# Kernel optimization log

Hardware: AMD Instinct MI355X
Metric: run time of the kernel (lower is better)

Reference implementation:

```python
import jax, jax.numpy as jnp
import numpy as np
from jax import lax

B, L, D = 2, 4096, 2048
K, KQ, M, H = 32, 4, 8, 8  # H = D*expand // (K*M)
MEM = K * H              # 256
FLAT = K * H * M         # 2048
CONV_W = 4
DIM_SWIGLU = H * 3 * 2   # out_expand_factor=3 -> 48
N_DECAY = K - 4          # 28 decay heads, 4 anchor heads


def setup_inputs() -> dict:
    key = jax.random.key(0)
    ks = jax.random.split(key, 8)
    x = jax.random.normal(ks[0], (B, L, D), dtype=jnp.float32)
    W_mem = jax.random.normal(ks[1], (D, MEM + K), dtype=jnp.float32) / np.sqrt(D)
    conv_k = jax.random.normal(ks[2], (CONV_W, 1, MEM + K), dtype=jnp.float32) * 0.3
    W_q = jax.random.normal(ks[3], (D, KQ * H * M * 2), dtype=jnp.float32) / np.sqrt(D)
    theta = jnp.asarray(np.tile(np.geomspace(0.001, 3.0, M).reshape(1, 1, 1, 1, M),
                                (1, 1, K, H, 1)), dtype=jnp.float32)
    decay_slopes = jnp.asarray(np.log(np.expm1(np.geomspace(0.001, 0.1, N_DECAY))), dtype=jnp.float32)
    anchor_slopes = jnp.asarray(np.log(np.expm1(np.geomspace(0.01, 0.1, 4))), dtype=jnp.float32)
    score_scale = jnp.ones((K,), dtype=jnp.float32)
    g = np.sqrt(2.0 / (H + DIM_SWIGLU))
    W_re = jax.random.normal(ks[4], (K, H, DIM_SWIGLU), dtype=jnp.float32) * g
    W_im = jax.random.normal(ks[5], (K, H, DIM_SWIGLU), dtype=jnp.float32) * g
    norm_scale = jnp.ones((1, 1, K, H), dtype=jnp.float32)
    W_out = jax.random.normal(ks[6], (K * H * 3, D), dtype=jnp.float32) / np.sqrt(K * H * 3)
    return {"x": x, "W_mem": W_mem, "conv_k": conv_k, "W_q": W_q, "theta": theta,
            "decay_slopes": decay_slopes, "anchor_slopes": anchor_slopes,
            "score_scale": score_scale, "W_re": W_re, "W_im": W_im,
            "norm_scale": norm_scale, "W_out": W_out}


def _forward(x, W_mem, conv_k, W_q, theta, decay_slopes, anchor_slopes,
             score_scale, W_re, W_im, norm_scale, W_out):
    b, l, d = x.shape
    # memory branch: dense + causal depthwise conv
    z = x @ W_mem  # (b, l, MEM+K)
    z = lax.conv_general_dilated(z, conv_k, window_strides=(1,),
                                 padding=[(CONV_W - 1, 0)],
                                 dimension_numbers=('NHC', 'HIO', 'NHC'),
                                 feature_group_count=MEM + K)
    k_val = z[..., :MEM].reshape(b, l, K, H)
    s_raw = z[..., MEM:].reshape(b, l, K, 1)
    # query branch
    q = (x @ W_q).reshape(b, l, KQ, H, M, 2)
    q_re, q_im = q[..., 0], q[..., 1]
    # per-head time weights (decay heads look back from end, anchor heads from start)
    pos = jnp.arange(l, dtype=jnp.float32)
    slopes_d = jax.nn.softplus(decay_slopes).reshape(1, 1, -1, 1)
    slopes_a = jax.nn.softplus(anchor_slopes).reshape(1, 1, -1, 1)
    dist = jnp.maximum(jnp.float32(l - 1) - pos, 0.0)
    log_w = jnp.concatenate([-slopes_d * dist[None, :, None, None],
                             -slopes_a * pos[None, :, None, None]], axis=2)  # (1,l,K,1)
    log_p = jnp.clip(score_scale[None, None, :, None] * s_raw, -20.0, 20.0)
    p_w = jnp.exp(log_p + log_w)  # (b,l,K,1)
    # complex rotation of keys
    phi = k_val[..., None] * theta          # (b,l,K,H,M)
    re_k, im_k = jnp.cos(phi), jnp.sin(phi)
    pw5 = p_w[..., None]
    merged = jnp.concatenate([p_w.squeeze(-1),
                              (pw5 * re_k).reshape(b, l, FLAT),
                              (pw5 * im_k).reshape(b, l, FLAT)], axis=-1)
    cs = jnp.cumsum(merged, axis=1)
    den = cs[..., :K]                       # (b,l,K)
    num_re = cs[..., K:K + FLAT]
    num_im = cs[..., K + FLAT:]
    inv_den = 1.0 / jnp.maximum(den[..., None], 1e-4)  # (b,l,K,1)
    state_re = num_re.reshape(b, l, K, H, M) * inv_den[..., None]
    state_im = num_im.reshape(b, l, K, H, M) * inv_den[..., None]
    # GQA-style query repeat
    n_rep = K // KQ
    q_re = jnp.repeat(q_re, n_rep, axis=2)
    q_im = jnp.repeat(q_im, n_rep, axis=2)
    out_re = jnp.sum(state_re * q_re + state_im * q_im, axis=-1)  # (b,l,K,H)
    out_im = jnp.sum(state_im * q_re - state_re * q_im, axis=-1)
    out_re = out_re * norm_scale
    out_im = out_im * norm_scale
    y = jnp.einsum('blkh,khn->blkn', out_re, W_re) + jnp.einsum('blkh,khn->blkn', out_im, W_im)
    y_val, y_gate = jnp.split(y, 2, axis=-1)
    y = (y_val * jax.nn.silu(y_gate)).reshape(b, l, -1)
    return y @ W_out


def reference(x, W_mem, conv_k, W_q, theta, decay_slopes, anchor_slopes,
              score_scale, W_re, W_im, norm_scale, W_out):
    return _forward(x, W_mem, conv_k, W_q, theta, decay_slopes, anchor_slopes,
                    score_scale, W_re, W_im, norm_scale, W_out)
```

## Files before the change

kernel.cpp:

```cpp
#include <hip/hip_runtime.h>
#include <hip/hip_bf16.h>
#include <math.h>

#define BB 2
#define LL 4096
#define DD 2048
#define KK 32
#define MEM 256
#define CTOT 288
#define NQ 512
#define ZSTR 800
#define NPAD 896
#define FLAT 2048
#define CMERG 4128
#define CH 16
#define NCH 256
#define YDIM 768
#define KV2 1536
#define BL (BB*LL)

typedef __attribute__((ext_vector_type(4))) float f32x4;
typedef __attribute__((ext_vector_type(8))) short bf16x8;
typedef __attribute__((ext_vector_type(8))) unsigned short u16x8;

__device__ inline unsigned short f2b(float v) {
    __hip_bfloat16 h = __float2bfloat16(v);
    return *reinterpret_cast<unsigned short*>(&h);
}
__device__ inline float b2f(unsigned short u) {
    __hip_bfloat16 h;
    *reinterpret_cast<unsigned short*>(&h) = u;
    return __bfloat162float(h);
}

__device__ inline void gload16(const void* g, void* l) {
    __builtin_amdgcn_global_load_lds(
        (const __attribute__((address_space(1))) unsigned int*)g,
        (__attribute__((address_space(3))) unsigned int*)l, 16, 0, 0);
}

template<int HH>
__device__ inline float bcast8(float v) {
    return __int_as_float(__builtin_amdgcn_ds_swizzle(__float_as_int(v), (HH << 5) | 0x18));
}

__device__ inline float fast_sigmoid_mul(float val, float g) {
    return val * __builtin_amdgcn_rcpf(1.f + __expf(-g));
}

__global__ __launch_bounds__(256) void cvt_x(const float* __restrict__ x,
                                             unsigned short* __restrict__ xb) {
    size_t i = ((size_t)blockIdx.x * 256 + threadIdx.x) * 8;
    float4 a = *(const float4*)&x[i];
    float4 b = *(const float4*)&x[i + 4];
    u16x8 o;
    o[0] = f2b(a.x); o[1] = f2b(a.y); o[2] = f2b(a.z); o[3] = f2b(a.w);
    o[4] = f2b(b.x); o[5] = f2b(b.y); o[6] = f2b(b.z); o[7] = f2b(b.w);
    *(u16x8*)&xb[i] = o;
}

__global__ __launch_bounds__(256) void prep_wb(const float* __restrict__ W_mem,
                                               const float* __restrict__ W_q,
                                               unsigned short* __restrict__ Wb) {
    int n = blockIdx.x;
    for (int k = threadIdx.x; k < DD; k += 256) {
        float v = 0.f;
        if (n < CTOT) v = W_mem[(size_t)k * CTOT + n];
        else if (n < ZSTR) v = W_q[(size_t)k * NQ + (n - CTOT)];
        Wb[(size_t)n * DD + k] = f2b(v);
    }
}

__global__ __launch_bounds__(256) void prep_wo(const float* __restrict__ W_out,
                                               unsigned short* __restrict__ Wo) {
    int n = blockIdx.x;
    for (int k = threadIdx.x; k < YDIM; k += 256) {
        float v = W_out[(size_t)k * DD + n];
        unsigned short hi = f2b(v);
        float r = v - b2f(hi);
        Wo[(size_t)n * KV2 + k] = hi;
        Wo[(size_t)n * KV2 + YDIM + k] = f2b(r);
    }
}

template<bool CBF16>
__global__ __launch_bounds__(256) void gemm_mfma(const unsigned short* __restrict__ A,
                                                 const unsigned short* __restrict__ Bh_g,
                                                 void* __restrict__ Cout,
                                                 int Kd, int Nvalid, int Cstride) {
    __shared__ unsigned short As[2][4096];
    __shared__ unsigned short Bh[2][4096];
    int tid = threadIdx.x;
    int lane = tid & 63;
    int wave = tid >> 6;
    int wr = wave >> 1, wc = wave & 1;

    int nwg = gridDim.x * gridDim.y;
    int bid = blockIdx.y * gridDim.x + blockIdx.x;
    int cpx = nwg >> 3;
    int swz = (bid & 7) * cpx + (bid >> 3);
    int bx = swz % gridDim.x, by = swz / gridDim.x;
    int m0 = by * 128;
    int n0 = bx * 128;

    f32x4 acc[4][4];
#pragma unroll
    for (int i = 0; i < 4; ++i)
#pragma unroll
        for (int j = 0; j < 4; ++j) acc[i][j] = (f32x4){0.f, 0.f, 0.f, 0.f};

    int f0 = tid, f1 = 256 + tid;
    int row0 = f0 >> 2, ks0 = (f0 & 3) ^ ((row0 >> 1) & 3);
    int row1 = f1 >> 2, ks1 = (f1 & 3) ^ ((row1 >> 1) & 3);
    const unsigned short* ga0 = &A[(size_t)(m0 + row0) * Kd + ks0 * 8];
    const unsigned short* ga1 = &A[(size_t)(m0 + row1) * Kd + ks1 * 8];
    const unsigned short* gb0 = &Bh_g[(size_t)(n0 + row0) * Kd + ks0 * 8];
    const unsigned short* gb1 = &Bh_g[(size_t)(n0 + row1) * Kd + ks1 * 8];
    int l0 = (wave * 64) * 8;
    int l1 = (256 + wave * 64) * 8;

    int g = lane >> 4, rr = lane & 15;

#define STAGE(buf, koff) do {                                          \
        gload16(ga0 + (koff), &As[buf][l0]);                           \
        gload16(ga1 + (koff), &As[buf][l1]);                           \
        gload16(gb0 + (koff), &Bh[buf][l0]);                           \
        gload16(gb1 + (koff), &Bh[buf][l1]);                           \
    } while (0)

    STAGE(0, 0);
    __syncthreads();

    int nIter = Kd >> 5;
    int cur = 0;
    for (int it = 0; it < nIter; ++it) {
        if (it + 1 < nIter) STAGE(cur ^ 1, (it + 1) * 32);

        bf16x8 av[4], bhv[4];
#pragma unroll
        for (int i = 0; i < 4; ++i) {
            int ra = wr * 64 + i * 16 + rr;
            av[i] = *(const bf16x8*)&As[cur][ra * 32 + ((g ^ ((ra >> 1) & 3)) * 8)];
            int rb = wc * 64 + i * 16 + rr;
            bhv[i] = *(const bf16x8*)&Bh[cur][rb * 32 + ((g ^ ((rb >> 1) & 3)) * 8)];
        }
#pragma unroll
        for (int i = 0; i < 4; ++i)
#pragma unroll
            for (int j = 0; j < 4; ++j)
                acc[i][j] = __builtin_amdgcn_mfma_f32_16x16x32_bf16(av[i], bhv[j], acc[i][j], 0, 0, 0);

        __syncthreads();
        cur ^= 1;
    }
#undef STAGE

    int cg = lane >> 4, cr = lane & 15;
#pragma unroll
    for (int i = 0; i < 4; ++i)
#pragma unroll
        for (int j = 0; j < 4; ++j) {
            int colb = n0 + wc * 64 + j * 16 + cr;
            if (colb < Nvalid) {
#pragma unroll
                for (int r = 0; r < 4; ++r) {
                    int rowb = m0 + wr * 64 + i * 16 + cg * 4 + r;
                    if (CBF16)
                        ((unsigned short*)Cout)[(size_t)rowb * Cstride + colb] = f2b(acc[i][j][r]);
                    else
                        ((float*)Cout)[(size_t)rowb * Cstride + colb] = acc[i][j][r];
                }
            }
        }
}

__global__ __launch_bounds__(512, 2) void gemm256(const unsigned short* __restrict__ A,
                                                  const unsigned short* __restrict__ Bm,
                                                  float* __restrict__ C,
                                                  int KA, int Kv, int Cstride) {
    __shared__ __attribute__((aligned(16))) unsigned short As[2][16384];
    __shared__ __attribute__((aligned(16))) unsigned short Bs[2][16384];
    int tid = threadIdx.x;
    int lane = tid & 63, wave = tid >> 6;
    int wm = wave >> 2, wn = wave & 3;

    int nwg = gridDim.x * gridDim.y;
    int bid = blockIdx.y * gridDim.x + blockIdx.x;
    int cpx = nwg >> 3;
    int swz = (bid & 7) * cpx + (bid >> 3);
    int bx = swz % gridDim.x, by = swz / gridDim.x;
    int m0 = by * 256, n0 = bx * 256;

    f32x4 acc[8][4];
#pragma unroll
    for (int i = 0; i < 8; ++i)
#pragma unroll
        for (int j = 0; j < 4; ++j) acc[i][j] = (f32x4){0.f, 0.f, 0.f, 0.f};

    const unsigned short* pA[4];
    const unsigned short* pB[4];
    int ldsoff[4];
#pragma unroll
    for (int j = 0; j < 4; ++j) {
        int f = j * 512 + tid;
        int row = f >> 3, s = f & 7;
        int sg = s ^ (row & 7);
        pA[j] = A + (size_t)(m0 + row) * KA + sg * 8;
        pB[j] = Bm + (size_t)(n0 + row) * Kv + sg * 8;
        ldsoff[j] = (j * 512 + wave * 64) * 8;
    }

    int rr = lane & 15, kg = lane >> 4;

#pragma unroll
    for (int j = 0; j < 4; ++j) gload16(pB[j], &Bs[0][ldsoff[j]]);
#pragma unroll
    for (int j = 0; j < 4; ++j) gload16(pA[j], &As[0][ldsoff[j]]);
    asm volatile("s_waitcnt vmcnt(0)" ::: "memory");
    __builtin_amdgcn_s_barrier();

    int nT = Kv >> 6;
    int cur = 0;

#define LDA(fr, t) ({ int ra_ = wm * 128 + (fr) * 16 + rr;                       \
        int sd_ = (t) * 4 + kg;                                                  \
        *(const bf16x8*)&As[cur][(ra_ * 8 + (sd_ ^ (ra_ & 7))) * 8]; })
#define LDB(fc, t) ({ int rb_ = wn * 64 + (fc) * 16 + rr;                        \
        int sd_ = (t) * 4 + kg;                                                  \
        *(const bf16x8*)&Bs[cur][(rb_ * 8 + (sd_ ^ (rb_ & 7))) * 8]; })

    for (int it = 0; it < nT; ++it) {
        int nxt = cur ^ 1;
        bool hn = (it + 1 < nT);
        int k0n = (it + 1) << 6;
        int kkA = (k0n >= KA) ? (k0n - KA) : k0n;

        if (hn) {
#pragma unroll
            for (int j = 0; j < 4; ++j) gload16(pB[j] + k0n, &Bs[nxt][ldsoff[j]]);
#pragma unroll
            for (int j = 0; j < 4; ++j) gload16(pA[j] + kkA, &As[nxt][ldsoff[j]]);
        }

        bf16x8 bv[8];
#pragma unroll
        for (int j = 0; j < 4; ++j) { bv[2 * j] = LDB(j, 0); bv[2 * j + 1] = LDB(j, 1); }
#pragma unroll
        for (int i = 0; i < 8; ++i) {
            bf16x8 a0 = LDA(i, 0);
            bf16x8 a1 = LDA(i, 1);
#pragma unroll
            for (int j = 0; j < 4; ++j) {
                acc[i][j] = __builtin_amdgcn_mfma_f32_16x16x32_bf16(a0, bv[2 * j], acc[i][j], 0, 0, 0);
                acc[i][j] = __builtin_amdgcn_mfma_f32_16x16x32_bf16(a1, bv[2 * j + 1], acc[i][j], 0, 0, 0);
            }
        }

        asm volatile("s_waitcnt vmcnt(0)" ::: "memory");
        __builtin_amdgcn_s_barrier();
        cur = nxt;
    }
#undef LDA
#undef LDB

    int cg = lane >> 4;
#pragma unroll
    for (int i = 0; i < 8; ++i)
#pragma unroll
        for (int j = 0; j < 4; ++j) {
            int colb = n0 + wn * 64 + j * 16 + rr;
#pragma unroll
            for (int r = 0; r < 4; ++r) {
                int rowb = m0 + wm * 128 + i * 16 + cg * 4 + r;
                C[(size_t)rowb * Cstride + colb] = acc[i][j][r];
            }
        }
}

__global__ __launch_bounds__(256) void fused_partial(const unsigned short* __restrict__ zq,
                                                     const float* __restrict__ conv_k,
                                                     const float* __restrict__ theta,
                                                     const float* __restrict__ decay,
                                                     const float* __restrict__ anchor,
                                                     const float* __restrict__ sscale,
                                                     float* __restrict__ partials) {
    int chunk = blockIdx.x, b = blockIdx.y, t = threadIdx.x;
    int l0 = chunk * CH;
    __shared__ unsigned short zin[CH + 3][CTOT];

    for (int idx = t; idx < (CH + 3) * 36; idx += 256) {
        int r = idx / 36, c8 = (idx % 36) * 8;
        int l = l0 - 3 + r;
        u16x8 v = (u16x8)(0);
        if (l >= 0) v = *(const u16x8*)&zq[(size_t)(b * LL + l) * ZSTR + c8];
        *(u16x8*)&zin[r][c8] = v;
    }
    __syncthreads();

    int k = t >> 3;
    float cz0 = conv_k[t], cz1 = conv_k[CTOT + t], cz2 = conv_k[2 * CTOT + t], cz3 = conv_k[3 * CTOT + t];
    int sc = MEM + k;
    float cs0 = conv_k[sc], cs1 = conv_k[CTOT + sc], cs2 = conv_k[2 * CTOT + sc], cs3 = conv_k[3 * CTOT + sc];
    float xx = (k < KK - 4) ? decay[k] : anchor[k - (KK - 4)];
    float sp = (xx > 20.f) ? xx : log1pf(__expf(xx));
    float ss = sscale[k];
    float th[8];
#pragma unroll
    for (int m = 0; m < 8; ++m) th[m] = theta[t * 8 + m];
    float rs[8], is[8];
#pragma unroll
    for (int m = 0; m < 8; ++m) { rs[m] = 0.f; is[m] = 0.f; }
    float dsum = 0.f;

#pragma unroll 1
    for (int i = 0; i < CH; ++i) {
        float kv = b2f(zin[i][t]) * cz0 + b2f(zin[i + 1][t]) * cz1 +
                   b2f(zin[i + 2][t]) * cz2 + b2f(zin[i + 3][t]) * cz3;
        float s = b2f(zin[i][sc]) * cs0 + b2f(zin[i + 1][sc]) * cs1 +
                  b2f(zin[i + 2][sc]) * cs2 + b2f(zin[i + 3][sc]) * cs3;
        int l = l0 + i;
        float lw = (k < KK - 4) ? -sp * (float)(LL - 1 - l) : -sp * (float)l;
        float lp = fminf(fmaxf(ss * s, -20.f), 20.f);
        float p = __expf(lp + lw);
        dsum += p;
#pragma unroll
        for (int m = 0; m < 8; ++m) {
            float sn, cn;
            __sincosf(kv * th[m], &sn, &cn);
            rs[m] += p * cn;
            is[m] += p * sn;
        }
    }
    size_t base = ((size_t)b * NCH + chunk) * CMERG;
    *(f32x4*)&partials[base + KK + t * 8]            = (f32x4){rs[0], rs[1], rs[2], rs[3]};
    *(f32x4*)&partials[base + KK + t * 8 + 4]        = (f32x4){rs[4], rs[5], rs[6], rs[7]};
    *(f32x4*)&partials[base + KK + FLAT + t * 8]     = (f32x4){is[0], is[1], is[2], is[3]};
    *(f32x4*)&partials[base + KK + FLAT + t * 8 + 4] = (f32x4){is[4], is[5], is[6], is[7]};
    if ((t & 7) == 0) partials[base + k] = dsum;
}

__global__ __launch_bounds__(256) void scan_partials(float* __restrict__ partials) {
    int t = threadIdx.x;
    int cl = t & 15, j = t >> 4;
    int c = blockIdx.x * 16 + cl;
    int b = blockIdx.y;
    float v[16];
    float s = 0.f;
#pragma unroll
    for (int i = 0; i < 16; ++i) {
        v[i] = partials[((size_t)b * NCH + j * 16 + i) * CMERG + c];
        s += v[i];
    }
    __shared__ float sums[16][17];
    sums[j][cl] = s;
    __syncthreads();
    if (j == 0) {
        float run = 0.f;
#pragma unroll
        for (int jj = 0; jj < 16; ++jj) {
            float x = sums[jj][cl];
            sums[jj][cl] = run;
            run += x;
        }
    }
    __syncthreads();
    float run = sums[j][cl];
#pragma unroll
    for (int i = 0; i < 16; ++i) {
        float x = v[i];
        partials[((size_t)b * NCH + j * 16 + i) * CMERG + c] = run;
        run += x;
    }
}

__global__ __launch_bounds__(256) void fused_stage(const unsigned short* __restrict__ zq,
                                                   const float* __restrict__ conv_k,
                                                   const float* __restrict__ theta,
                                                   const float* __restrict__ decay,
                                                   const float* __restrict__ anchor,
                                                   const float* __restrict__ sscale,
                                                   const float* __restrict__ partials,
                                                   const float* __restrict__ W_re,
                                                   const float* __restrict__ W_im,
                                                   const float* __restrict__ nscale,
                                                   unsigned short* __restrict__ y_act) {
    int chunk = blockIdx.x, b = blockIdx.y, t = threadIdx.x;
    int l0 = chunk * CH;
    __shared__ unsigned short zin[CH + 3][CTOT];
    __shared__ unsigned short qall[CH][NQ];

    for (int idx = t; idx < (CH + 3) * 36; idx += 256) {
        int r = idx / 36, c8 = (idx % 36) * 8;
        int l = l0 - 3 + r;
        u16x8 v = (u16x8)(0);
        if (l >= 0) v = *(const u16x8*)&zq[(size_t)(b * LL + l) * ZSTR + c8];
        *(u16x8*)&zin[r][c8] = v;
    }
    for (int idx = t; idx < CH * (NQ / 8); idx += 256) {
        int i = idx >> 6, c8 = (idx & 63) * 8;
        *(u16x8*)&qall[i][c8] = *(const u16x8*)&zq[(size_t)(b * LL + l0 + i) * ZSTR + CTOT + c8];
    }
    __syncthreads();

    int k = t >> 3, h = t & 7, w = t >> 6;
    float cz0 = conv_k[t], cz1 = conv_k[CTOT + t], cz2 = conv_k[2 * CTOT + t], cz3 = conv_k[3 * CTOT + t];
    int sc = MEM + k;
    float cs0 = conv_k[sc], cs1 = conv_k[CTOT + sc], cs2 = conv_k[2 * CTOT + sc], cs3 = conv_k[3 * CTOT + sc];
    float xx = (k < KK - 4) ? decay[k] : anchor[k - (KK - 4)];
    float sp = (xx > 20.f) ? xx : log1pf(__expf(xx));
    float ss = sscale[k];
    float th[8];
#pragma unroll
    for (int m = 0; m < 8; ++m) th[m] = theta[t * 8 + m];
    float ns = nscale[t];
    int qb = w * 128 + h * 16;

    float wre[8][6], wim[8][6];
#pragma unroll
    for (int hh = 0; hh < 8; ++hh)
#pragma unroll
        for (int jj = 0; jj < 6; ++jj) {
            wre[hh][jj] = W_re[(k * 8 + hh) * 48 + h + 8 * jj];
            wim[hh][jj] = W_im[(k * 8 + hh) * 48 + h + 8 * jj];
        }

    size_t pbase = ((size_t)b * NCH + chunk) * CMERG;
    f32x4 r0 = *(const f32x4*)&partials[pbase + KK + t * 8];
    f32x4 r1 = *(const f32x4*)&partials[pbase + KK + t * 8 + 4];
    f32x4 i0 = *(const f32x4*)&partials[pbase + KK + FLAT + t * 8];
    f32x4 i1 = *(const f32x4*)&partials[pbase + KK + FLAT + t * 8 + 4];
    float rs[8] = {r0[0], r0[1], r0[2], r0[3], r1[0], r1[1], r1[2], r1[3]};
    float is[8] = {i0[0], i0[1], i0[2], i0[3], i1[0], i1[1], i1[2], i1[3]};
    float den = partials[pbase + k];

#pragma unroll 1
    for (int i = 0; i < CH; ++i) {
        float kv = b2f(zin[i][t]) * cz0 + b2f(zin[i + 1][t]) * cz1 +
                   b2f(zin[i + 2][t]) * cz2 + b2f(zin[i + 3][t]) * cz3;
        float s = b2f(zin[i][sc]) * cs0 + b2f(zin[i + 1][sc]) * cs1 +
                  b2f(zin[i + 2][sc]) * cs2 + b2f(zin[i + 3][sc]) * cs3;
        int l = l0 + i;
        float lw = (k < KK - 4) ? -sp * (float)(LL - 1 - l) : -sp * (float)l;
        float lp = fminf(fmaxf(ss * s, -20.f), 20.f);
        float p = __expf(lp + lw);
        den += p;
        float inv = __builtin_amdgcn_rcpf(fmaxf(den, 1e-4f));
#pragma unroll
        for (int m = 0; m < 8; ++m) {
            float sn, cn;
            __sincosf(kv * th[m], &sn, &cn);
            rs[m] += p * cn;
            is[m] += p * sn;
        }
        u16x8 qv0 = *(const u16x8*)&qall[i][qb];
        u16x8 qv1 = *(const u16x8*)&qall[i][qb + 8];
        float o_re = 0.f, o_im = 0.f;
#pragma unroll
        for (int m = 0; m < 8; ++m) {
            float sre = rs[m] * inv;
            float sim = is[m] * inv;
            float qre = b2f((unsigned short)((m < 4) ? qv0[2 * m] : qv1[2 * m - 8]));
            float qim = b2f((unsigned short)((m < 4) ? qv0[2 * m + 1] : qv1[2 * m - 7]));
            o_re += sre * qre + sim * qim;
            o_im += sim * qre - sre * qim;
        }
        o_re *= ns;
        o_im *= ns;

        float y0 = 0.f, y1 = 0.f, y2 = 0.f, y3 = 0.f, y4 = 0.f, y5 = 0.f;
#define EAPPLY(HH) { float br_ = bcast8<HH>(o_re); float bi_ = bcast8<HH>(o_im); \
        y0 += br_ * wre[HH][0] + bi_ * wim[HH][0]; \
        y1 += br_ * wre[HH][1] + bi_ * wim[HH][1]; \
        y2 += br_ * wre[HH][2] + bi_ * wim[HH][2]; \
        y3 += br_ * wre[HH][3] + bi_ * wim[HH][3]; \
        y4 += br_ * wre[HH][4] + bi_ * wim[HH][4]; \
        y5 += br_ * wre[HH][5] + bi_ * wim[HH][5]; }
        EAPPLY(0) EAPPLY(1) EAPPLY(2) EAPPLY(3)
        EAPPLY(4) EAPPLY(5) EAPPLY(6) EAPPLY(7)
#undef EAPPLY

        size_t ybase = (size_t)(b * LL + l) * YDIM + k * 24 + h;
        y_act[ybase]      = f2b(fast_sigmoid_mul(y0 * y3, y3));
        y_act[ybase + 8]  = f2b(fast_sigmoid_mul(y1 * y4, y4));
        y_act[ybase + 16] = f2b(fast_sigmoid_mul(y2 * y5, y5));
    }
}

extern "C" void kernel_launch(void* const* d_in, const int* in_sizes, int n_in,
                              void* d_out, int out_size, void* d_ws, size_t ws_size,
                              hipStream_t stream) {
    const float* x      = (const float*)d_in[0];
    const float* W_mem  = (const float*)d_in[1];
    const float* conv_k = (const float*)d_in[2];
    const float* W_q    = (const float*)d_in[3];
    const float* theta  = (const float*)d_in[4];
    const float* decay  = (const float*)d_in[5];
    const float* anchor = (const float*)d_in[6];
    const float* sscale = (const float*)d_in[7];
    const float* W_re   = (const float*)d_in[8];
    const float* W_im   = (const float*)d_in[9];
    const float* nscale = (const float*)d_in[10];
    const float* W_out  = (const float*)d_in[11];
    float* out = (float*)d_out;
    float* ws = (float*)d_ws;

    unsigned short* xb = (unsigned short*)out;
    unsigned short* Wb = (unsigned short*)(out + 8388608);
    unsigned short* zq = (unsigned short*)(out + 9306112);
    float* partials      = ws;
    unsigned short* yb   = (unsigned short*)(ws + 2113536);
    unsigned short* Wo   = (unsigned short*)(ws + 5259264);

    cvt_x<<<8192, 256, 0, stream>>>(x, xb);
    prep_wb<<<NPAD, 256, 0, stream>>>(W_mem, W_q, Wb);
    prep_wo<<<DD, 256, 0, stream>>>(W_out, Wo);

    gemm_mfma<true><<<dim3(NPAD / 128, BL / 128), 256, 0, stream>>>(
        xb, Wb, zq, DD, ZSTR, ZSTR);
    fused_partial<<<dim3(NCH, BB), 256, 0, stream>>>(zq, conv_k, theta, decay, anchor, sscale, partials);
    scan_partials<<<dim3(CMERG / 16, BB), 256, 0, stream>>>(partials);
    fused_stage<<<dim3(NCH, BB), 256, 0, stream>>>(zq, conv_k, theta, decay, anchor, sscale,
                                                   partials, W_re, W_im, nscale, yb);
    gemm256<<<dim3(DD / 256, BL / 256), 512, 0, stream>>>(yb, Wo, out, YDIM, KV2, DD);
}
```

Baseline: 183.1 us.

## Fuse fp32-to-bf16 x conversion into first GEMM and drop split-bf16 W_out

Removes the separate cvt_x kernel by having the first GEMM load fp32 x directly, convert it to bf16 in registers and store it to LDS, overlapping the global loads with MFMA work. It also drops the hi/lo bf16 split of W_out, which halves the K dimension of the output GEMM. This saves one full pass over x and half of the final GEMM's work. The cost is lower precision on W_out and a register-staged A path in place of direct global-to-LDS loads.

```diff
diff --git a/kernel.cpp b/kernel.cpp
--- a/kernel.cpp
+++ b/kernel.cpp
@@ -16,7 +16,6 @@
 #define CH 16
 #define NCH 256
 #define YDIM 768
-#define KV2 1536
 #define BL (BB*LL)
 
 typedef __attribute__((ext_vector_type(4))) float f32x4;
@@ -39,6 +38,13 @@
         (__attribute__((address_space(3))) unsigned int*)l, 16, 0, 0);
 }
 
+__device__ inline u16x8 cvt8(float4 a, float4 b) {
+    u16x8 o;
+    o[0] = f2b(a.x); o[1] = f2b(a.y); o[2] = f2b(a.z); o[3] = f2b(a.w);
+    o[4] = f2b(b.x); o[5] = f2b(b.y); o[6] = f2b(b.z); o[7] = f2b(b.w);
+    return o;
+}
+
 template<int HH>
 __device__ inline float bcast8(float v) {
     return __int_as_float(__builtin_amdgcn_ds_swizzle(__float_as_int(v), (HH << 5) | 0x18));
@@ -46,17 +52,6 @@
 
 __device__ inline float fast_sigmoid_mul(float val, float g) {
     return val * __builtin_amdgcn_rcpf(1.f + __expf(-g));
-}
-
-__global__ __launch_bounds__(256) void cvt_x(const float* __restrict__ x,
-                                             unsigned short* __restrict__ xb) {
-    size_t i = ((size_t)blockIdx.x * 256 + threadIdx.x) * 8;
-    float4 a = *(const float4*)&x[i];
-    float4 b = *(const float4*)&x[i + 4];
-    u16x8 o;
-    o[0] = f2b(a.x); o[1] = f2b(a.y); o[2] = f2b(a.z); o[3] = f2b(a.w);
-    o[4] = f2b(b.x); o[5] = f2b(b.y); o[6] = f2b(b.z); o[7] = f2b(b.w);
-    *(u16x8*)&xb[i] = o;
 }
 
 __global__ __launch_bounds__(256) void prep_wb(const float* __restrict__ W_mem,
@@ -75,19 +70,14 @@
                                                unsigned short* __restrict__ Wo) {
     int n = blockIdx.x;
     for (int k = threadIdx.x; k < YDIM; k += 256) {
-        float v = W_out[(size_t)k * DD + n];
-        unsigned short hi = f2b(v);
-        float r = v - b2f(hi);
-        Wo[(size_t)n * KV2 + k] = hi;
-        Wo[(size_t)n * KV2 + YDIM + k] = f2b(r);
-    }
-}
-
-template<bool CBF16>
-__global__ __launch_bounds__(256) void gemm_mfma(const unsigned short* __restrict__ A,
-                                                 const unsigned short* __restrict__ Bh_g,
-                                                 void* __restrict__ Cout,
-                                                 int Kd, int Nvalid, int Cstride) {
+        Wo[(size_t)n * YDIM + k] = f2b(W_out[(size_t)k * DD + n]);
+    }
+}
+
+__global__ __launch_bounds__(256) void gemm_zq(const float* __restrict__ Af,
+                                               const unsigned short* __restrict__ Bh_g,
+                                               unsigned short* __restrict__ Cout,
+                                               int Kd, int Nvalid, int Cstride) {
     __shared__ unsigned short As[2][4096];
     __shared__ unsigned short Bh[2][4096];
     int tid = threadIdx.x;
@@ -112,8 +102,8 @@
     int f0 = tid, f1 = 256 + tid;
     int row0 = f0 >> 2, ks0 = (f0 & 3) ^ ((row0 >> 1) & 3);
     int row1 = f1 >> 2, ks1 = (f1 & 3) ^ ((row1 >> 1) & 3);
-    const unsigned short* ga0 = &A[(size_t)(m0 + row0) * Kd + ks0 * 8];
-    const unsigned short* ga1 = &A[(size_t)(m0 + row1) * Kd + ks1 * 8];
+    const float* ga0 = &Af[(size_t)(m0 + row0) * Kd + ks0 * 8];
+    const float* ga1 = &Af[(size_t)(m0 + row1) * Kd + ks1 * 8];
     const unsigned short* gb0 = &Bh_g[(size_t)(n0 + row0) * Kd + ks0 * 8];
     const unsigned short* gb1 = &Bh_g[(size_t)(n0 + row1) * Kd + ks1 * 8];
     int l0 = (wave * 64) * 8;
@@ -121,20 +111,29 @@
 
     int g = lane >> 4, rr = lane & 15;
 
-#define STAGE(buf, koff) do {                                          \
-        gload16(ga0 + (koff), &As[buf][l0]);                           \
-        gload16(ga1 + (koff), &As[buf][l1]);                           \
-        gload16(gb0 + (koff), &Bh[buf][l0]);                           \
-        gload16(gb1 + (koff), &Bh[buf][l1]);                           \
-    } while (0)
-
-    STAGE(0, 0);
+    {
+        gload16(gb0, &Bh[0][l0]);
+        gload16(gb1, &Bh[0][l1]);
+        float4 p00 = *(const float4*)(ga0), p01 = *(const float4*)(ga0 + 4);
+        float4 p10 = *(const float4*)(ga1), p11 = *(const float4*)(ga1 + 4);
+        *(u16x8*)&As[0][f0 * 8] = cvt8(p00, p01);
+        *(u16x8*)&As[0][f1 * 8] = cvt8(p10, p11);
+    }
     __syncthreads();
 
     int nIter = Kd >> 5;
     int cur = 0;
     for (int it = 0; it < nIter; ++it) {
-        if (it + 1 < nIter) STAGE(cur ^ 1, (it + 1) * 32);
+        int nxt = cur ^ 1;
+        bool hn = (it + 1 < nIter);
+        int k0n = (it + 1) * 32;
+        float4 p00, p01, p10, p11;
+        if (hn) {
+            gload16(gb0 + k0n, &Bh[nxt][l0]);
+            gload16(gb1 + k0n, &Bh[nxt][l1]);
+            p00 = *(const float4*)(ga0 + k0n); p01 = *(const float4*)(ga0 + k0n + 4);
+            p10 = *(const float4*)(ga1 + k0n); p11 = *(const float4*)(ga1 + k0n + 4);
+        }
 
         bf16x8 av[4], bhv[4];
 #pragma unroll
@@ -150,10 +149,13 @@
             for (int j = 0; j < 4; ++j)
                 acc[i][j] = __builtin_amdgcn_mfma_f32_16x16x32_bf16(av[i], bhv[j], acc[i][j], 0, 0, 0);
 
+        if (hn) {
+            *(u16x8*)&As[nxt][f0 * 8] = cvt8(p00, p01);
+            *(u16x8*)&As[nxt][f1 * 8] = cvt8(p10, p11);
+        }
         __syncthreads();
-        cur ^= 1;
-    }
-#undef STAGE
+        cur = nxt;
+    }
 
     int cg = lane >> 4, cr = lane & 15;
 #pragma unroll
@@ -165,10 +167,7 @@
 #pragma unroll
                 for (int r = 0; r < 4; ++r) {
                     int rowb = m0 + wr * 64 + i * 16 + cg * 4 + r;
-                    if (CBF16)
-                        ((unsigned short*)Cout)[(size_t)rowb * Cstride + colb] = f2b(acc[i][j][r]);
-                    else
-                        ((float*)Cout)[(size_t)rowb * Cstride + colb] = acc[i][j][r];
+                    Cout[(size_t)rowb * Cstride + colb] = f2b(acc[i][j][r]);
                 }
             }
         }
@@ -177,7 +176,7 @@
 __global__ __launch_bounds__(512, 2) void gemm256(const unsigned short* __restrict__ A,
                                                   const unsigned short* __restrict__ Bm,
                                                   float* __restrict__ C,
-                                                  int KA, int Kv, int Cstride) {
+                                                  int Kd, int Cstride) {
     __shared__ __attribute__((aligned(16))) unsigned short As[2][16384];
     __shared__ __attribute__((aligned(16))) unsigned short Bs[2][16384];
     int tid = threadIdx.x;
@@ -205,8 +204,8 @@
         int f = j * 512 + tid;
         int row = f >> 3, s = f & 7;
         int sg = s ^ (row & 7);
-        pA[j] = A + (size_t)(m0 + row) * KA + sg * 8;
-        pB[j] = Bm + (size_t)(n0 + row) * Kv + sg * 8;
+        pA[j] = A + (size_t)(m0 + row) * Kd + sg * 8;
+        pB[j] = Bm + (size_t)(n0 + row) * Kd + sg * 8;
         ldsoff[j] = (j * 512 + wave * 64) * 8;
     }
 
@@ -219,7 +218,7 @@
     asm volatile("s_waitcnt vmcnt(0)" ::: "memory");
     __builtin_amdgcn_s_barrier();
 
-    int nT = Kv >> 6;
+    int nT = Kd >> 6;
     int cur = 0;
 
 #define LDA(fr, t) ({ int ra_ = wm * 128 + (fr) * 16 + rr;                       \
@@ -233,13 +232,12 @@
         int nxt = cur ^ 1;
         bool hn = (it + 1 < nT);
         int k0n = (it + 1) << 6;
-        int kkA = (k0n >= KA) ? (k0n - KA) : k0n;
 
         if (hn) {
 #pragma unroll
             for (int j = 0; j < 4; ++j) gload16(pB[j] + k0n, &Bs[nxt][ldsoff[j]]);
 #pragma unroll
-            for (int j = 0; j < 4; ++j) gload16(pA[j] + kkA, &As[nxt][ldsoff[j]]);
+            for (int j = 0; j < 4; ++j) gload16(pA[j] + k0n, &As[nxt][ldsoff[j]]);
         }
 
         bf16x8 bv[8];
@@ -504,22 +502,20 @@
     float* out = (float*)d_out;
     float* ws = (float*)d_ws;
 
-    unsigned short* xb = (unsigned short*)out;
-    unsigned short* Wb = (unsigned short*)(out + 8388608);
-    unsigned short* zq = (unsigned short*)(out + 9306112);
+    unsigned short* Wb = (unsigned short*)out;
+    unsigned short* zq = (unsigned short*)(out + 917504);
     float* partials      = ws;
     unsigned short* yb   = (unsigned short*)(ws + 2113536);
     unsigned short* Wo   = (unsigned short*)(ws + 5259264);
 
-    cvt_x<<<8192, 256, 0, stream>>>(x, xb);
     prep_wb<<<NPAD, 256, 0, stream>>>(W_mem, W_q, Wb);
     prep_wo<<<DD, 256, 0, stream>>>(W_out, Wo);
 
-    gemm_mfma<true><<<dim3(NPAD / 128, BL / 128), 256, 0, stream>>>(
-        xb, Wb, zq, DD, ZSTR, ZSTR);
+    gemm_zq<<<dim3(NPAD / 128, BL / 128), 256, 0, stream>>>(
+        x, Wb, zq, DD, ZSTR, ZSTR);
     fused_partial<<<dim3(NCH, BB), 256, 0, stream>>>(zq, conv_k, theta, decay, anchor, sscale, partials);
     scan_partials<<<dim3(CMERG / 16, BB), 256, 0, stream>>>(partials);
     fused_stage<<<dim3(NCH, BB), 256, 0, stream>>>(zq, conv_k, theta, decay, anchor, sscale,
                                                    partials, W_re, W_im, nscale, yb);
-    gemm256<<<dim3(DD / 256, BL / 256), 512, 0, stream>>>(yb, Wo, out, YDIM, KV2, DD);
-}
+    gemm256<<<dim3(DD / 256, BL / 256), 512, 0, stream>>>(yb, Wo, out, YDIM, DD);
+}
```

After: 174.2 us. -4.9%, faster.
